# Kernel tuning notes

Measured on AMD Instinct MI355X. Metric: run time of the kernel, lower is better.

Reference implementation:

```python
import jax, jax.numpy as jnp
import numpy as np
from jax import lax

DN = ('NCHW', 'OIHW', 'NCHW')


def conv2d(x, w, b, stride, pad):
    y = lax.conv_general_dilated(x, w, (stride, stride), [(pad, pad), (pad, pad)],
                                 dimension_numbers=DN)
    return y + b[None, :, None, None]


def conv_transpose2d_k4s2p1(x, w, b):
    # torch ConvTranspose2d(k=4, s=2, p=1); w is torch layout [Cin, Cout, 4, 4].
    # Equivalent forward conv: lhs_dilation=2, pad = k-1-p = 2, spatially-flipped kernel.
    k = jnp.flip(w, (2, 3)).transpose(1, 0, 2, 3)  # -> OIHW [Cout, Cin, 4, 4]
    y = lax.conv_general_dilated(x, k, (1, 1), [(2, 2), (2, 2)],
                                 lhs_dilation=(2, 2), dimension_numbers=DN)
    return y + b[None, :, None, None]


def setup_inputs() -> dict:
    key = jax.random.key(0)
    ks = jax.random.split(key, 16)

    def w(k, shape):
        fan_in = int(np.prod(shape[1:]))
        return jax.random.normal(k, shape, jnp.float32) * np.float32(1.0 / np.sqrt(fan_in))

    inp = {}
    inp['x'] = jax.random.uniform(ks[0], (256, 1, 128, 128), jnp.float32)
    # Encoder
    inp['enc_w1'] = w(ks[1], (32, 1, 4, 4));   inp['enc_b1'] = jnp.zeros((32,), jnp.float32)
    inp['enc_w2'] = w(ks[2], (64, 32, 4, 4));  inp['enc_b2'] = jnp.zeros((64,), jnp.float32)
    inp['enc_w3'] = w(ks[3], (64, 64, 3, 3));  inp['enc_b3'] = jnp.zeros((64,), jnp.float32)
    inp['enc_w4'] = w(ks[4], (32, 64, 1, 1));  inp['enc_b4'] = jnp.zeros((32,), jnp.float32)
    # Codebook: uniform(-sqrt(3/512), sqrt(3/512))
    mx = np.float32(np.sqrt(3.0 / 512.0))
    inp['codebook'] = jax.random.uniform(ks[5], (512, 32), jnp.float32, -mx, mx)
    # Decoder
    inp['dec_w1'] = w(ks[6], (64, 32, 3, 3));  inp['dec_b1'] = jnp.zeros((64,), jnp.float32)
    inp['dect_w1'] = w(ks[7], (64, 32, 4, 4)); inp['dect_b1'] = jnp.zeros((32,), jnp.float32)  # torch [Cin,Cout,k,k]
    inp['dect_w2'] = w(ks[8], (32, 1, 4, 4));  inp['dect_b2'] = jnp.zeros((1,), jnp.float32)
    return inp


def vqvae_forward(x, enc_w1, enc_b1, enc_w2, enc_b2, enc_w3, enc_b3, enc_w4, enc_b4,
                  codebook, dec_w1, dec_b1, dect_w1, dect_b1, dect_w2, dect_b2):
    # Encoder: 128 -> 64 -> 32 spatial, 32 channels out
    h = jax.nn.relu(conv2d(x, enc_w1, enc_b1, 2, 1))
    h = jax.nn.relu(conv2d(h, enc_w2, enc_b2, 2, 1))
    h = jax.nn.relu(conv2d(h, enc_w3, enc_b3, 1, 1))
    z = conv2d(h, enc_w4, enc_b4, 1, 0)            # [B, 32, 32, 32]

    # Vector quantization (NCHW -> NHWC -> flat)
    zin = jnp.moveaxis(z, 1, -1)                   # [B, H, W, D]
    flat = zin.reshape(-1, zin.shape[-1])          # [N, D]
    dists = (jnp.sum(flat * flat, -1, keepdims=True)
             + jnp.sum(codebook * codebook, -1)
             - 2.0 * flat @ codebook.T)            # [N, K]
    idx = jnp.argmin(dists, -1)                    # [N]
    quant = codebook[idx].reshape(zin.shape)       # == one_hot @ codebook

    emb_loss = jnp.mean((quant - lax.stop_gradient(zin)) ** 2)
    com_loss = 0.26 * jnp.mean((lax.stop_gradient(quant) - zin) ** 2)
    vq_loss = emb_loss + com_loss
    quant = zin + lax.stop_gradient(quant - zin)   # straight-through
    qz = jnp.moveaxis(quant, -1, 1)                # [B, 32, 32, 32]

    # Decoder: 32 -> 64 -> 128 spatial
    d = jax.nn.relu(conv2d(qz, dec_w1, dec_b1, 1, 1))
    d = jax.nn.relu(conv_transpose2d_k4s2p1(d, dect_w1, dect_b1))
    recon = jax.nn.sigmoid(conv_transpose2d_k4s2p1(d, dect_w2, dect_b2))
    return recon, vq_loss


def reference(x, enc_w1, enc_b1, enc_w2, enc_b2, enc_w3, enc_b3, enc_w4, enc_b4,
              codebook, dec_w1, dec_b1, dect_w1, dect_b1, dect_w2, dect_b2):
    return vqvae_forward(x, enc_w1, enc_b1, enc_w2, enc_b2, enc_w3, enc_b3, enc_w4, enc_b4,
                         codebook, dec_w1, dec_b1, dect_w1, dect_b1, dect_w2, dect_b2)
```

## Files before the change

kernel.cpp:

```cpp
#include <hip/hip_runtime.h>
#include <math.h>

typedef __attribute__((ext_vector_type(8))) short short8;
typedef __attribute__((ext_vector_type(4))) float f32x4;

__device__ inline unsigned short f2bf(float f) {
  unsigned u = __float_as_uint(f);
  u = (u + 0x7fffu + ((u >> 16) & 1u)) >> 16;
  return (unsigned short)u;
}

__global__ __launch_bounds__(256, 3)
void conv1_lds(const float* __restrict__ x, const float* __restrict__ w,
               const float* __restrict__ bias, float* __restrict__ out) {
  int bid = blockIdx.x;
  int cchunk = bid & 1;
  int t4 = (bid >> 1) & 3;
  int n = bid >> 3;
  int co0 = cchunk * 16;
  int y0 = t4 * 16;
  int yi0 = 2 * y0 - 1;

  __shared__ float xs[34 * 128];
  __shared__ float wl[16][16];

  int t = threadIdx.x;
  for (int idx = t; idx < 34 * 128; idx += 256) {
    int gy = yi0 + (idx >> 7);
    int gx = idx & 127;
    bool ok = (unsigned)gy < 128;
    xs[idx] = ok ? x[(size_t)n * 16384 + gy * 128 + gx] : 0.f;
  }
  {
    int cc = t & 15;
    int tap = t >> 4;
    if (t < 256) wl[tap][cc] = w[(size_t)(co0 + cc) * 16 + tap];
  }
  __syncthreads();

  int sx = t & 63;
  int rg = t >> 6;

  float acc[4][16];
#pragma unroll
  for (int j = 0; j < 4; j++)
#pragma unroll
    for (int c = 0; c < 16; c++) acc[j][c] = 0.f;

  int ix0 = 2 * sx - 1;
#pragma unroll
  for (int ky = 0; ky < 4; ky++) {
#pragma unroll
    for (int kx = 0; kx < 4; kx++) {
      int ix = ix0 + kx;
      bool xok = (unsigned)ix < 128;
      float xv[4];
#pragma unroll
      for (int j = 0; j < 4; j++) {
        int lrow = 2 * (4 * rg + j) + ky;
        float v = xs[lrow * 128 + (xok ? ix : 0)];
        xv[j] = xok ? v : 0.f;
      }
      const float* wr = &wl[ky * 4 + kx][0];
#pragma unroll
      for (int c = 0; c < 16; c += 4) {
        float4 wv = *(const float4*)(wr + c);
#pragma unroll
        for (int j = 0; j < 4; j++) {
          acc[j][c + 0] = fmaf(xv[j], wv.x, acc[j][c + 0]);
          acc[j][c + 1] = fmaf(xv[j], wv.y, acc[j][c + 1]);
          acc[j][c + 2] = fmaf(xv[j], wv.z, acc[j][c + 2]);
          acc[j][c + 3] = fmaf(xv[j], wv.w, acc[j][c + 3]);
        }
      }
    }
  }

#pragma unroll
  for (int j = 0; j < 4; j++) {
    int oy = y0 + 4 * rg + j;
    float* op = out + (((size_t)n * 32 + co0) * 64 + oy) * 64 + sx;
#pragma unroll
    for (int c = 0; c < 16; c++) {
      float v = acc[j][c] + bias[co0 + c];
      op[(size_t)c * 4096] = fmaxf(v, 0.f);
    }
  }
}

template<int CIN, int COUT, int CCH>
__global__ __launch_bounds__(256, 3)
void conv4x4s2_lds(const float* __restrict__ x, const float* __restrict__ w,
                   const float* __restrict__ bias, float* __restrict__ out) {
  constexpr int NCH = COUT / CCH;
  int bid = blockIdx.x;
  int cchunk = bid % NCH;
  int n = bid / NCH;
  int co0 = cchunk * CCH;

  __shared__ float wl[CIN * 16][CCH];
  __shared__ float xs[4096];
  for (int i = threadIdx.x; i < CIN * 16 * CCH; i += 256) {
    int cc = i % CCH;
    int tap = i / CCH;
    wl[tap][cc] = w[(size_t)(co0 + cc) * (CIN * 16) + tap];
  }

  int t = threadIdx.x;
  int sx = t & 31;
  int sy0 = t >> 5;
  int ix0 = 2 * sx - 1;

  float acc[4][CCH];
#pragma unroll
  for (int j = 0; j < 4; j++)
#pragma unroll
    for (int c = 0; c < CCH; c++) acc[j][c] = 0.f;

  const float* xn = x + (size_t)n * CIN * 4096;

  for (int ci = 0; ci < CIN; ci++) {
    __syncthreads();
#pragma unroll
    for (int k = 0; k < 4; k++)
      *(float4*)(xs + k * 1024 + t * 4) =
          *(const float4*)(xn + (size_t)ci * 4096 + k * 1024 + t * 4);
    __syncthreads();

#pragma unroll
    for (int ky = 0; ky < 4; ky++) {
#pragma unroll
      for (int kx = 0; kx < 4; kx++) {
        int ix = ix0 + kx;
        bool xok = (unsigned)ix < 64;
        float xv[4];
#pragma unroll
        for (int j = 0; j < 4; j++) {
          int iy = 2 * (sy0 + j * 8) - 1 + ky;
          bool ok = xok && ((unsigned)iy < 64);
          float v = xs[ok ? iy * 64 + ix : 0];
          xv[j] = ok ? v : 0.f;
        }
        const float* wr = &wl[ci * 16 + ky * 4 + kx][0];
#pragma unroll
        for (int c = 0; c < CCH; c += 4) {
          float4 wv = *(const float4*)(wr + c);
#pragma unroll
          for (int j = 0; j < 4; j++) {
            acc[j][c + 0] = fmaf(xv[j], wv.x, acc[j][c + 0]);
            acc[j][c + 1] = fmaf(xv[j], wv.y, acc[j][c + 1]);
            acc[j][c + 2] = fmaf(xv[j], wv.z, acc[j][c + 2]);
            acc[j][c + 3] = fmaf(xv[j], wv.w, acc[j][c + 3]);
          }
        }
      }
    }
  }

#pragma unroll
  for (int j = 0; j < 4; j++) {
    int sy = sy0 + j * 8;
    float* op = out + (((size_t)n * COUT + co0) * 32 + sy) * 32 + sx;
#pragma unroll
    for (int c = 0; c < CCH; c++) {
      float v = acc[j][c] + bias[co0 + c];
      v = fmaxf(v, 0.f);
      op[(size_t)c * 1024] = v;
    }
  }
}

template<int CIN, int COUT, int CCH>
__global__ __launch_bounds__(256, 3)
void conv3x3_cg(const float* __restrict__ x, const float* __restrict__ w,
                const float* __restrict__ bias, float* __restrict__ out) {
  constexpr int NCH = COUT / CCH;
  int bid = blockIdx.x;
  int cchunk = bid % NCH;
  int n = bid / NCH;
  int co0 = cchunk * CCH;

  __shared__ float xs[4 * 1024];
  __shared__ float wl[4 * 9][CCH];

  int t = threadIdx.x;
  int sx = t & 31;
  int rg = t >> 5;

  float acc[4][CCH];
#pragma unroll
  for (int j = 0; j < 4; j++)
#pragma unroll
    for (int c = 0; c < CCH; c++) acc[j][c] = 0.f;

  const float* xn = x + (size_t)n * CIN * 1024;

  for (int cg = 0; cg < CIN / 4; cg++) {
    __syncthreads();
#pragma unroll
    for (int k = 0; k < 4; k++)
      *(float4*)(xs + k * 1024 + t * 4) =
          *(const float4*)(xn + (size_t)(cg * 4 + k) * 1024 + t * 4);
    for (int i = t; i < 4 * 9 * CCH; i += 256) {
      int cc = i % CCH;
      int row = i / CCH;
      int c4 = row / 9, kk = row % 9;
      wl[row][cc] = w[(size_t)(co0 + cc) * (CIN * 9) + (cg * 4 + c4) * 9 + kk];
    }
    __syncthreads();

#pragma unroll
    for (int c4 = 0; c4 < 4; c4++) {
      const float* xc = xs + c4 * 1024;
      float xv[6][3];
#pragma unroll
      for (int r = 0; r < 6; r++) {
        int iy = 4 * rg - 1 + r;
        bool yok = (unsigned)iy < 32;
#pragma unroll
        for (int cx = 0; cx < 3; cx++) {
          int ix = sx - 1 + cx;
          bool ok = yok && ((unsigned)ix < 32);
          float v = xc[ok ? iy * 32 + ix : 0];
          xv[r][cx] = ok ? v : 0.f;
        }
      }
#pragma unroll
      for (int ky = 0; ky < 3; ky++) {
#pragma unroll
        for (int kx = 0; kx < 3; kx++) {
          const float* wr = &wl[c4 * 9 + ky * 3 + kx][0];
#pragma unroll
          for (int c = 0; c < CCH; c += 4) {
            float4 wv = *(const float4*)(wr + c);
#pragma unroll
            for (int j = 0; j < 4; j++) {
              float xx = xv[j + ky][kx];
              acc[j][c + 0] = fmaf(xx, wv.x, acc[j][c + 0]);
              acc[j][c + 1] = fmaf(xx, wv.y, acc[j][c + 1]);
              acc[j][c + 2] = fmaf(xx, wv.z, acc[j][c + 2]);
              acc[j][c + 3] = fmaf(xx, wv.w, acc[j][c + 3]);
            }
          }
        }
      }
    }
  }

#pragma unroll
  for (int j = 0; j < 4; j++) {
    int sy = 4 * rg + j;
    float* op = out + (((size_t)n * COUT + co0) * 32 + sy) * 32 + sx;
#pragma unroll
    for (int c = 0; c < CCH; c++) {
      float v = acc[j][c] + bias[co0 + c];
      v = fmaxf(v, 0.f);
      op[(size_t)c * 1024] = v;
    }
  }
}

__global__ void wprep_dect1(const float* __restrict__ tw1,
                            unsigned short* __restrict__ Bws) {
  int i = blockIdx.x * 256 + threadIdx.x;
  if (i < 32768) {
    int ci = i & 63;
    int co = (i >> 6) & 31;
    int tap = (i >> 11) & 3;
    int par = i >> 13;
    int py = par >> 1, px = par & 1;
    int ky0 = (py + 1) & 1, kx0 = (px + 1) & 1;
    int kyi = tap >> 1, kxi = tap & 1;
    int ky = ky0 + 2 * kyi, kx = kx0 + 2 * kxi;
    Bws[i] = f2bf(tw1[(((size_t)ci * 32 + co) * 4 + ky) * 4 + kx]);
  }
}

__global__ void wprep_dec1(const float* __restrict__ dw1,
                           unsigned short* __restrict__ Wd1) {
  int i = blockIdx.x * 256 + threadIdx.x;
  if (i < 18432) {
    int ci = i & 31;
    int tap = (i >> 5) % 9;
    int co = i / 288;
    Wd1[i] = f2bf(dw1[(size_t)(co * 32 + ci) * 9 + tap]);
  }
}

__global__ __launch_bounds__(256, 3)
void dec1_mfma(const float* __restrict__ qz,
               const unsigned short* __restrict__ Wd1,
               const float* __restrict__ bias, float* __restrict__ d1) {
  int strip = blockIdx.x & 3;
  int smp = blockIdx.x >> 2;
  int y0 = strip * 8;

  __shared__ __align__(16) unsigned short xt[10 * 34 * 32];

  int t = threadIdx.x;
  for (int idx = t; idx < 16 * 10 * 34; idx += 256) {
    int cc = idx % 34;
    int tmp = idx / 34;
    int rr = tmp % 10;
    int pp = tmp / 10;
    int gy = y0 - 1 + rr;
    int gx = cc - 1;
    bool ok = ((unsigned)gy < 32) && ((unsigned)gx < 32);
    const float* p = qz + ((size_t)smp * 32 + 2 * pp) * 1024 + gy * 32 + gx;
    float v0 = ok ? p[0] : 0.f;
    float v1 = ok ? p[1024] : 0.f;
    unsigned pk = (unsigned)f2bf(v0) | ((unsigned)f2bf(v1) << 16);
    *(unsigned*)(&xt[(rr * 34 + cc) * 32 + 2 * pp]) = pk;
  }

  int lane = t & 63;
  int wv = t >> 6;
  int mlo = lane & 15;
  int khi = lane >> 4;

  short8 afr[9];
#pragma unroll
  for (int tap = 0; tap < 9; tap++)
    afr[tap] = *(const short8*)(Wd1 + (size_t)(wv * 16 + mlo) * 288 +
                                tap * 32 + khi * 8);
  float bb[4];
#pragma unroll
  for (int r = 0; r < 4; r++) bb[r] = bias[wv * 16 + khi * 4 + r];

  __syncthreads();

  for (int pt = 0; pt < 16; pt++) {
    int rl = pt >> 1;
    int chf = pt & 1;
    f32x4 acc = {0.f, 0.f, 0.f, 0.f};
#pragma unroll
    for (int tap = 0; tap < 9; tap++) {
      int ky = tap / 3, kx = tap % 3;
      const unsigned short* bp =
          xt + (((rl + ky) * 34) + chf * 16 + mlo + kx) * 32 + khi * 8;
      short8 b = *(const short8*)bp;
      acc = __builtin_amdgcn_mfma_f32_16x16x32_bf16(afr[tap], b, acc, 0, 0, 0);
    }
    int gyo = y0 + rl;
    int gxo = chf * 16 + mlo;
#pragma unroll
    for (int r = 0; r < 4; r++) {
      int co = wv * 16 + khi * 4 + r;
      d1[(((size_t)smp * 64 + co) * 32 + gyo) * 32 + gxo] =
          fmaxf(acc[r] + bb[r], 0.f);
    }
  }
}

__global__ __launch_bounds__(256, 3)
void convt_mfma(const float* __restrict__ d1,
                const unsigned short* __restrict__ Bws,
                const float* __restrict__ bias, float* __restrict__ d2) {
  constexpr int CP = 72;
  int bid = blockIdx.x;
  int rp = bid & 15;
  int smp = bid >> 4;

  __shared__ __align__(16) unsigned short xt[4 * 34 * CP];

  int t = threadIdx.x;

  for (int idx = t; idx < 32 * 4 * 34; idx += 256) {
    int cc = idx % 34;
    int tmp = idx / 34;
    int rr = tmp & 3;
    int pp = tmp >> 2;
    int gy = 2 * rp - 1 + rr;
    int gx = cc - 1;
    bool ok = ((unsigned)gy < 32) && ((unsigned)gx < 32);
    const float* p = d1 + ((size_t)smp * 64 + 2 * pp) * 1024 + gy * 32 + gx;
    float v0 = ok ? p[0] : 0.f;
    float v1 = ok ? p[1024] : 0.f;
    unsigned pk = (unsigned)f2bf(v0) | ((unsigned)f2bf(v1) << 16);
    *(unsigned*)(&xt[(rr * 34 + cc) * CP + 2 * pp]) = pk;
  }
  __syncthreads();

  int lane = t & 63;
  int wv = t >> 6;
  int row2 = wv >> 1;
  int c0 = (wv & 1) * 16;
  int mlo = lane & 15;
  int khi = lane >> 4;

  f32x4 acc[4][2];
#pragma unroll
  for (int par = 0; par < 4; par++)
#pragma unroll
    for (int nt = 0; nt < 2; nt++) {
      f32x4 z = {0.f, 0.f, 0.f, 0.f};
      acc[par][nt] = z;
    }

#pragma unroll
  for (int par = 0; par < 4; par++) {
    int py = par >> 1, px = par & 1;
    int ky0 = (py + 1) & 1, kx0 = (px + 1) & 1;
    int ay = (py + 1 - ky0) >> 1;
    int ax = (px + 1 - kx0) >> 1;
#pragma unroll
    for (int tap = 0; tap < 4; tap++) {
      int kyi = tap >> 1, kxi = tap & 1;
      int rrp = row2 + 1 + (ay - kyi);
      int ccb = c0 + 1 + (ax - kxi);
#pragma unroll
      for (int kc = 0; kc < 2; kc++) {
        const unsigned short* ap =
            xt + ((rrp * 34) + ccb + mlo) * CP + kc * 32 + khi * 8;
        short8 a = *(const short8*)ap;
#pragma unroll
        for (int nt = 0; nt < 2; nt++) {
          const unsigned short* bp =
              Bws + (((size_t)(par * 4 + tap) * 32 + nt * 16 + mlo) * 64) +
              kc * 32 + khi * 8;
          short8 b = *(const short8*)bp;
          acc[par][nt] =
              __builtin_amdgcn_mfma_f32_16x16x32_bf16(a, b, acc[par][nt], 0, 0, 0);
        }
      }
    }
  }

  int sy = 2 * rp + row2;
#pragma unroll
  for (int par = 0; par < 4; par++) {
    int py = par >> 1, px = par & 1;
    int oy = 2 * sy + py;
#pragma unroll
    for (int nt = 0; nt < 2; nt++) {
      int co = nt * 16 + mlo;
      float b = bias[co];
      float* op = d2 + (((size_t)smp * 32 + co) * 64 + oy) * 64;
#pragma unroll
      for (int r = 0; r < 4; r++) {
        int sx = c0 + khi * 4 + r;
        int ox = 2 * sx + px;
        op[ox] = fmaxf(acc[par][nt][r] + b, 0.f);
      }
    }
  }
}

__global__ __launch_bounds__(256, 4)
void dect2_full(const float* __restrict__ x, const float* __restrict__ w,
                const float* __restrict__ bias, float* __restrict__ out) {
  int ptile = blockIdx.x & 3;
  int n = blockIdx.x >> 2;
  int y0 = ptile * 16;

  __shared__ float xs[8][1152];
  int t = threadIdx.x;
  int sx = t & 63;
  int r4 = t >> 6;

  float acc[4][4];
#pragma unroll
  for (int j = 0; j < 4; j++)
#pragma unroll
    for (int p = 0; p < 4; p++) acc[j][p] = 0.f;

  const float* xn = x + (size_t)n * 32 * 4096;

  for (int cg = 0; cg < 4; cg++) {
    __syncthreads();
    for (int idx = t; idx < 8 * 1152; idx += 256) {
      int ch = idx / 1152;
      int rem = idx % 1152;
      int iy = y0 - 1 + rem / 64;
      int ix = rem & 63;
      bool ok = (unsigned)iy < 64;
      xs[ch][rem] = ok ? xn[(size_t)(cg * 8 + ch) * 4096 + iy * 64 + ix] : 0.f;
    }
    __syncthreads();

#pragma unroll
    for (int c4 = 0; c4 < 8; c4++) {
      int ci = cg * 8 + c4;
      const float* xc = &xs[c4][0];
      float xv[6][3];
#pragma unroll
      for (int r = 0; r < 6; r++) {
        int srow = 4 * r4 + r;
#pragma unroll
        for (int cx = 0; cx < 3; cx++) {
          int ix = sx - 1 + cx;
          bool ok = (unsigned)ix < 64;
          float v = xc[ok ? srow * 64 + ix : 0];
          xv[r][cx] = ok ? v : 0.f;
        }
      }
      float w16[16];
#pragma unroll
      for (int q = 0; q < 4; q++) {
        float4 ww = *(const float4*)(w + ci * 16 + 4 * q);
        w16[4 * q + 0] = ww.x; w16[4 * q + 1] = ww.y;
        w16[4 * q + 2] = ww.z; w16[4 * q + 3] = ww.w;
      }
#pragma unroll
      for (int py = 0; py < 2; py++) {
#pragma unroll
        for (int px = 0; px < 2; px++) {
          int par = py * 2 + px;
          int ky0 = (py + 1) & 1, kx0 = (px + 1) & 1;
          int ay = (py + 1 - ky0) >> 1;
          int ax = (px + 1 - kx0) >> 1;
#pragma unroll
          for (int kyi = 0; kyi < 2; kyi++) {
#pragma unroll
            for (int kxi = 0; kxi < 2; kxi++) {
              float wv = w16[(ky0 + 2 * kyi) * 4 + (kx0 + 2 * kxi)];
#pragma unroll
              for (int j = 0; j < 4; j++) {
                float xx = xv[j + ay + 1 - kyi][ax + 1 - kxi];
                acc[j][par] = fmaf(xx, wv, acc[j][par]);
              }
            }
          }
        }
      }
    }
  }

  float b0 = bias[0];
#pragma unroll
  for (int j = 0; j < 4; j++) {
    int iy = y0 + 4 * r4 + j;
#pragma unroll
    for (int py = 0; py < 2; py++) {
      float v0 = acc[j][py * 2 + 0] + b0;
      float v1 = acc[j][py * 2 + 1] + b0;
      float2 o;
      o.x = 1.f / (1.f + expf(-v0));
      o.y = 1.f / (1.f + expf(-v1));
      int oy = 2 * iy + py;
      *(float2*)(out + (size_t)n * 16384 + oy * 128 + 2 * sx) = o;
    }
  }
}

__global__ void cbn_prep(const float* __restrict__ cb, float* __restrict__ cbn) {
#pragma clang fp contract(off)
  int k = blockIdx.x * 256 + threadIdx.x;
  if (k < 512) {
    float m[32];
#pragma unroll
    for (int d = 0; d < 32; d++) {
      float c = cb[k * 32 + d];
      m[d] = c * c;
    }
    float r[8];
#pragma unroll
    for (int j = 0; j < 8; j++)
      r[j] = ((m[j] + m[8 + j]) + m[16 + j]) + m[24 + j];
    cbn[k] = ((r[0] + r[1]) + (r[2] + r[3])) + ((r[4] + r[5]) + (r[6] + r[7]));
  }
}

__global__ __launch_bounds__(256)
void vq_fused(const float* __restrict__ h3, const float* __restrict__ w4,
              const float* __restrict__ b4, const float* __restrict__ cb,
              const float* __restrict__ cbn, float* __restrict__ qz,
              float* __restrict__ loss) {
  __shared__ float wl[64][32];
  int tid = threadIdx.x;
  for (int i = tid; i < 2048; i += 256) {
    int co = i & 31;
    int ci = i >> 5;
    wl[ci][co] = w4[(size_t)co * 64 + ci];
  }
  __syncthreads();

  int n = blockIdx.x >> 2;
  int p = (blockIdx.x & 3) * 256 + tid;
  const float* hn = h3 + (size_t)n * 65536;

  float zv[32];
#pragma unroll
  for (int c = 0; c < 32; c++) zv[c] = 0.f;
  for (int ci = 0; ci < 64; ci++) {
    float xv = hn[(size_t)ci * 1024 + p];
#pragma unroll
    for (int c = 0; c < 32; c += 4) {
      float4 wv = *(const float4*)&wl[ci][c];
      zv[c + 0] = fmaf(xv, wv.x, zv[c + 0]);
      zv[c + 1] = fmaf(xv, wv.y, zv[c + 1]);
      zv[c + 2] = fmaf(xv, wv.z, zv[c + 2]);
      zv[c + 3] = fmaf(xv, wv.w, zv[c + 3]);
    }
  }
#pragma unroll
  for (int c = 0; c < 32; c++) zv[c] = zv[c] + b4[c];

  float zz;
  {
#pragma clang fp contract(off)
    float m[32];
#pragma unroll
    for (int d = 0; d < 32; d++) m[d] = zv[d] * zv[d];
    float r[8];
#pragma unroll
    for (int j = 0; j < 8; j++)
      r[j] = ((m[j] + m[8 + j]) + m[16 + j]) + m[24 + j];
    zz = ((r[0] + r[1]) + (r[2] + r[3])) + ((r[4] + r[5]) + (r[6] + r[7]));
  }

  float best = 3.4e38f;
  int bk = 0;
  for (int k4 = 0; k4 < 512; k4 += 4) {
    float4 cn = *(const float4*)(cbn + k4);
    float da[4];
#pragma unroll
    for (int u = 0; u < 4; u++) da[u] = 0.f;
#pragma unroll
    for (int d = 0; d < 32; d += 4) {
#pragma unroll
      for (int u = 0; u < 4; u++) {
        float4 c = *(const float4*)(cb + (size_t)(k4 + u) * 32 + d);
        float a = da[u];
        a = fmaf(zv[d + 0], c.x, a);
        a = fmaf(zv[d + 1], c.y, a);
        a = fmaf(zv[d + 2], c.z, a);
        a = fmaf(zv[d + 3], c.w, a);
        da[u] = a;
      }
    }
#pragma unroll
    for (int u = 0; u < 4; u++) {
      float cnu = (u == 0) ? cn.x : (u == 1) ? cn.y : (u == 2) ? cn.z : cn.w;
      float s;
      {
#pragma clang fp contract(off)
        s = (zz + cnu) - 2.f * da[u];
      }
      int k = k4 + u;
      if (s < best) { best = s; bk = k; }
    }
  }

  float lsum = 0.f;
  float* qn = qz + (size_t)n * 32768;
#pragma unroll
  for (int d = 0; d < 32; d += 4) {
#pragma clang fp contract(off)
    float4 q = *(const float4*)(cb + (size_t)bk * 32 + d);
    float e;
    e = q.x - zv[d + 0]; lsum = fmaf(e, e, lsum);
    e = q.y - zv[d + 1]; lsum = fmaf(e, e, lsum);
    e = q.z - zv[d + 2]; lsum = fmaf(e, e, lsum);
    e = q.w - zv[d + 3]; lsum = fmaf(e, e, lsum);
    qn[(size_t)(d + 0) * 1024 + p] = zv[d + 0] + (q.x - zv[d + 0]);
    qn[(size_t)(d + 1) * 1024 + p] = zv[d + 1] + (q.y - zv[d + 1]);
    qn[(size_t)(d + 2) * 1024 + p] = zv[d + 2] + (q.z - zv[d + 2]);
    qn[(size_t)(d + 3) * 1024 + p] = zv[d + 3] + (q.w - zv[d + 3]);
  }

#pragma unroll
  for (int off = 32; off; off >>= 1) lsum += __shfl_down(lsum, off, 64);
  if ((tid & 63) == 0) atomicAdd(loss, lsum);
}

__global__ void finalize_loss(const float* __restrict__ loss, float* __restrict__ out) {
  if (threadIdx.x == 0) {
    float m = loss[0] / 8388608.f;
    out[0] = m + 0.26f * m;
  }
}

extern "C" void kernel_launch(void* const* d_in, const int* in_sizes, int n_in,
                              void* d_out, int out_size, void* d_ws, size_t ws_size,
                              hipStream_t stream) {
  (void)in_sizes; (void)n_in; (void)out_size;
  const float* x   = (const float*)d_in[0];
  const float* ew1 = (const float*)d_in[1];
  const float* eb1 = (const float*)d_in[2];
  const float* ew2 = (const float*)d_in[3];
  const float* eb2 = (const float*)d_in[4];
  const float* ew3 = (const float*)d_in[5];
  const float* eb3 = (const float*)d_in[6];
  const float* ew4 = (const float*)d_in[7];
  const float* eb4 = (const float*)d_in[8];
  const float* cb  = (const float*)d_in[9];
  const float* dw1 = (const float*)d_in[10];
  const float* db1 = (const float*)d_in[11];
  const float* tw1 = (const float*)d_in[12];
  const float* tb1 = (const float*)d_in[13];
  const float* tw2 = (const float*)d_in[14];
  const float* tb2 = (const float*)d_in[15];
  float* out = (float*)d_out;

  auto need = [](size_t c) -> size_t {
    return (c * 196608 + 516 + 16384 + 9216) * 4;
  };
  int nchunks = 4;
  if (ws_size >= need(256)) nchunks = 1;
  else if (ws_size >= need(128)) nchunks = 2;
  int chunk = 256 / nchunks;

  float* ws = (float*)d_ws;
  float* A = ws;
  float* B = A + (size_t)chunk * 131072;
  float* cbn = B + (size_t)chunk * 65536;
  float* lossacc = cbn + 512;
  unsigned short* Bws = (unsigned short*)(cbn + 516);
  unsigned short* Wd1 = (unsigned short*)(cbn + 516 + 16384);

  float* h1 = A;
  float* h2 = B;
  float* h3 = A;
  float* qz = A + (size_t)chunk * 98304;
  float* d1 = B;
  float* d2 = A;

  cbn_prep<<<2, 256, 0, stream>>>(cb, cbn);
  wprep_dect1<<<128, 256, 0, stream>>>(tw1, Bws);
  wprep_dec1<<<72, 256, 0, stream>>>(dw1, Wd1);
  (void)hipMemsetAsync(lossacc, 0, 4, stream);

  for (int c = 0; c < nchunks; c++) {
    const float* xc = x + (size_t)c * chunk * 128 * 128;
    float* outc = out + (size_t)c * chunk * 128 * 128;

    conv1_lds<<<chunk * 8, 256, 0, stream>>>(xc, ew1, eb1, h1);
    conv4x4s2_lds<32, 64, 16>
        <<<chunk * 4, 256, 0, stream>>>(h1, ew2, eb2, h2);
    conv3x3_cg<64, 64, 16>
        <<<chunk * 4, 256, 0, stream>>>(h2, ew3, eb3, h3);

    vq_fused<<<chunk * 4, 256, 0, stream>>>(h3, ew4, eb4, cb, cbn, qz, lossacc);

    dec1_mfma<<<chunk * 4, 256, 0, stream>>>(qz, Wd1, db1, d1);
    convt_mfma<<<chunk * 16, 256, 0, stream>>>(d1, Bws, tb1, d2);
    dect2_full<<<chunk * 4, 256, 0, stream>>>(d2, tw2, tb2, outc);
  }

  finalize_loss<<<1, 64, 0, stream>>>(lossacc, out + 4194304);
}
```

Baseline: 1.085 ms.

## Enlarge per-block channel tile and per-thread register tile in encoder convs

The two middle encoder convolutions now give each block 32 output channels instead of 16, with each thread holding an 8-row by 16-channel accumulator tile, which halves the grid. Each staged input tile is therefore reused across twice as many output channels, and loaded weights across more rows, cutting global and LDS traffic per FMA. The 4x4 conv now stages only the current input channel's weights into a small LDS array each iteration instead of the whole weight slice up front. In exchange, register pressure rises (launch bounds drop to 2 blocks per SM) and the grid has fewer blocks, which lowers occupancy and latency hiding.

```diff
diff --git a/kernel.cpp b/kernel.cpp
--- a/kernel.cpp
+++ b/kernel.cpp
@@ -88,34 +88,30 @@
   }
 }
 
-template<int CIN, int COUT, int CCH>
-__global__ __launch_bounds__(256, 3)
-void conv4x4s2_lds(const float* __restrict__ x, const float* __restrict__ w,
-                   const float* __restrict__ bias, float* __restrict__ out) {
-  constexpr int NCH = COUT / CCH;
+template<int CIN, int COUT>
+__global__ __launch_bounds__(256, 2)
+void conv4x4s2_v2(const float* __restrict__ x, const float* __restrict__ w,
+                  const float* __restrict__ bias, float* __restrict__ out) {
+  constexpr int NCH = COUT / 32;
   int bid = blockIdx.x;
   int cchunk = bid % NCH;
   int n = bid / NCH;
-  int co0 = cchunk * CCH;
-
-  __shared__ float wl[CIN * 16][CCH];
+  int co0 = cchunk * 32;
+
   __shared__ float xs[4096];
-  for (int i = threadIdx.x; i < CIN * 16 * CCH; i += 256) {
-    int cc = i % CCH;
-    int tap = i / CCH;
-    wl[tap][cc] = w[(size_t)(co0 + cc) * (CIN * 16) + tap];
-  }
+  __shared__ float wl[16][32];
 
   int t = threadIdx.x;
   int sx = t & 31;
-  int sy0 = t >> 5;
+  int rg = (t >> 5) & 3;
+  int cob = (t >> 7) * 16;
   int ix0 = 2 * sx - 1;
 
-  float acc[4][CCH];
-#pragma unroll
-  for (int j = 0; j < 4; j++)
-#pragma unroll
-    for (int c = 0; c < CCH; c++) acc[j][c] = 0.f;
+  float acc[8][16];
+#pragma unroll
+  for (int j = 0; j < 8; j++)
+#pragma unroll
+    for (int c = 0; c < 16; c++) acc[j][c] = 0.f;
 
   const float* xn = x + (size_t)n * CIN * 4096;
 
@@ -125,6 +121,14 @@
     for (int k = 0; k < 4; k++)
       *(float4*)(xs + k * 1024 + t * 4) =
           *(const float4*)(xn + (size_t)ci * 4096 + k * 1024 + t * 4);
+    {
+      int i = t;
+      int cc = i & 31, tap = i >> 5;
+      wl[tap][cc] = w[(size_t)(co0 + cc) * (CIN * 16) + ci * 16 + tap];
+      i += 256;
+      cc = i & 31; tap = i >> 5;
+      wl[tap][cc] = w[(size_t)(co0 + cc) * (CIN * 16) + ci * 16 + tap];
+    }
     __syncthreads();
 
 #pragma unroll
@@ -133,20 +137,20 @@
       for (int kx = 0; kx < 4; kx++) {
         int ix = ix0 + kx;
         bool xok = (unsigned)ix < 64;
-        float xv[4];
-#pragma unroll
-        for (int j = 0; j < 4; j++) {
-          int iy = 2 * (sy0 + j * 8) - 1 + ky;
+        float xv[8];
+#pragma unroll
+        for (int j = 0; j < 8; j++) {
+          int iy = 2 * (8 * rg + j) - 1 + ky;
           bool ok = xok && ((unsigned)iy < 64);
           float v = xs[ok ? iy * 64 + ix : 0];
           xv[j] = ok ? v : 0.f;
         }
-        const float* wr = &wl[ci * 16 + ky * 4 + kx][0];
-#pragma unroll
-        for (int c = 0; c < CCH; c += 4) {
+        const float* wr = &wl[ky * 4 + kx][cob];
+#pragma unroll
+        for (int c = 0; c < 16; c += 4) {
           float4 wv = *(const float4*)(wr + c);
 #pragma unroll
-          for (int j = 0; j < 4; j++) {
+          for (int j = 0; j < 8; j++) {
             acc[j][c + 0] = fmaf(xv[j], wv.x, acc[j][c + 0]);
             acc[j][c + 1] = fmaf(xv[j], wv.y, acc[j][c + 1]);
             acc[j][c + 2] = fmaf(xv[j], wv.z, acc[j][c + 2]);
@@ -158,40 +162,40 @@
   }
 
 #pragma unroll
-  for (int j = 0; j < 4; j++) {
-    int sy = sy0 + j * 8;
-    float* op = out + (((size_t)n * COUT + co0) * 32 + sy) * 32 + sx;
-#pragma unroll
-    for (int c = 0; c < CCH; c++) {
-      float v = acc[j][c] + bias[co0 + c];
-      v = fmaxf(v, 0.f);
-      op[(size_t)c * 1024] = v;
-    }
-  }
-}
-
-template<int CIN, int COUT, int CCH>
-__global__ __launch_bounds__(256, 3)
-void conv3x3_cg(const float* __restrict__ x, const float* __restrict__ w,
+  for (int j = 0; j < 8; j++) {
+    int sy = 8 * rg + j;
+    float* op = out + (((size_t)n * COUT + co0 + cob) * 32 + sy) * 32 + sx;
+#pragma unroll
+    for (int c = 0; c < 16; c++) {
+      float v = acc[j][c] + bias[co0 + cob + c];
+      op[(size_t)c * 1024] = fmaxf(v, 0.f);
+    }
+  }
+}
+
+template<int CIN, int COUT>
+__global__ __launch_bounds__(256, 2)
+void conv3x3_v2(const float* __restrict__ x, const float* __restrict__ w,
                 const float* __restrict__ bias, float* __restrict__ out) {
-  constexpr int NCH = COUT / CCH;
+  constexpr int NCH = COUT / 32;
   int bid = blockIdx.x;
   int cchunk = bid % NCH;
   int n = bid / NCH;
-  int co0 = cchunk * CCH;
+  int co0 = cchunk * 32;
 
   __shared__ float xs[4 * 1024];
-  __shared__ float wl[4 * 9][CCH];
+  __shared__ float wl[4 * 9][32];
 
   int t = threadIdx.x;
   int sx = t & 31;
-  int rg = t >> 5;
-
-  float acc[4][CCH];
-#pragma unroll
-  for (int j = 0; j < 4; j++)
-#pragma unroll
-    for (int c = 0; c < CCH; c++) acc[j][c] = 0.f;
+  int rg = (t >> 5) & 3;
+  int cob = (t >> 7) * 16;
+
+  float acc[8][16];
+#pragma unroll
+  for (int j = 0; j < 8; j++)
+#pragma unroll
+    for (int c = 0; c < 16; c++) acc[j][c] = 0.f;
 
   const float* xn = x + (size_t)n * CIN * 1024;
 
@@ -201,9 +205,9 @@
     for (int k = 0; k < 4; k++)
       *(float4*)(xs + k * 1024 + t * 4) =
           *(const float4*)(xn + (size_t)(cg * 4 + k) * 1024 + t * 4);
-    for (int i = t; i < 4 * 9 * CCH; i += 256) {
-      int cc = i % CCH;
-      int row = i / CCH;
+    for (int i = t; i < 4 * 9 * 32; i += 256) {
+      int cc = i & 31;
+      int row = i >> 5;
       int c4 = row / 9, kk = row % 9;
       wl[row][cc] = w[(size_t)(co0 + cc) * (CIN * 9) + (cg * 4 + c4) * 9 + kk];
     }
@@ -212,10 +216,10 @@
 #pragma unroll
     for (int c4 = 0; c4 < 4; c4++) {
       const float* xc = xs + c4 * 1024;
-      float xv[6][3];
-#pragma unroll
-      for (int r = 0; r < 6; r++) {
-        int iy = 4 * rg - 1 + r;
+      float xv[10][3];
+#pragma unroll
+      for (int r = 0; r < 10; r++) {
+        int iy = 8 * rg - 1 + r;
         bool yok = (unsigned)iy < 32;
 #pragma unroll
         for (int cx = 0; cx < 3; cx++) {
@@ -229,12 +233,12 @@
       for (int ky = 0; ky < 3; ky++) {
 #pragma unroll
         for (int kx = 0; kx < 3; kx++) {
-          const float* wr = &wl[c4 * 9 + ky * 3 + kx][0];
-#pragma unroll
-          for (int c = 0; c < CCH; c += 4) {
+          const float* wr = &wl[c4 * 9 + ky * 3 + kx][cob];
+#pragma unroll
+          for (int c = 0; c < 16; c += 4) {
             float4 wv = *(const float4*)(wr + c);
 #pragma unroll
-            for (int j = 0; j < 4; j++) {
+            for (int j = 0; j < 8; j++) {
               float xx = xv[j + ky][kx];
               acc[j][c + 0] = fmaf(xx, wv.x, acc[j][c + 0]);
               acc[j][c + 1] = fmaf(xx, wv.y, acc[j][c + 1]);
@@ -248,14 +252,13 @@
   }
 
 #pragma unroll
-  for (int j = 0; j < 4; j++) {
-    int sy = 4 * rg + j;
-    float* op = out + (((size_t)n * COUT + co0) * 32 + sy) * 32 + sx;
-#pragma unroll
-    for (int c = 0; c < CCH; c++) {
-      float v = acc[j][c] + bias[co0 + c];
-      v = fmaxf(v, 0.f);
-      op[(size_t)c * 1024] = v;
+  for (int j = 0; j < 8; j++) {
+    int sy = 8 * rg + j;
+    float* op = out + (((size_t)n * COUT + co0 + cob) * 32 + sy) * 32 + sx;
+#pragma unroll
+    for (int c = 0; c < 16; c++) {
+      float v = acc[j][c] + bias[co0 + cob + c];
+      op[(size_t)c * 1024] = fmaxf(v, 0.f);
     }
   }
 }
@@ -726,10 +729,10 @@
     float* outc = out + (size_t)c * chunk * 128 * 128;
 
     conv1_lds<<<chunk * 8, 256, 0, stream>>>(xc, ew1, eb1, h1);
-    conv4x4s2_lds<32, 64, 16>
-        <<<chunk * 4, 256, 0, stream>>>(h1, ew2, eb2, h2);
-    conv3x3_cg<64, 64, 16>
-        <<<chunk * 4, 256, 0, stream>>>(h2, ew3, eb3, h3);
+    conv4x4s2_v2<32, 64>
+        <<<chunk * 2, 256, 0, stream>>>(h1, ew2, eb2, h2);
+    conv3x3_v2<64, 64>
+        <<<chunk * 2, 256, 0, stream>>>(h2, ew3, eb3, h3);
 
     vq_fused<<<chunk * 4, 256, 0, stream>>>(h3, ew4, eb4, cb, cbn, qz, lossacc);
 
```

Result: slower. 1.432 ms (+32.0%).

## Pad LDS halos, stream per-channel weights, raise occupancy bounds

Applied to the files above, without the earlier changes.

The conv4x4 encoder kernel now loads weights one input channel at a time into a small LDS tile instead of staging all CIN*16*CCH weights up front. Both encoder convs gain zeroed halo rows in LDS, so vertical bounds checks drop out of the inner loops. Launch bounds on several kernels go from 3 to 4 blocks per CU. The aim is lower LDS and register pressure for higher occupancy and cheaper indexing, at the cost of per-iteration weight loads from global memory and possible register spills under the tighter bound.

```diff
diff --git a/kernel.cpp b/kernel.cpp
--- a/kernel.cpp
+++ b/kernel.cpp
@@ -10,7 +10,7 @@
   return (unsigned short)u;
 }
 
-__global__ __launch_bounds__(256, 3)
+__global__ __launch_bounds__(256, 4)
 void conv1_lds(const float* __restrict__ x, const float* __restrict__ w,
                const float* __restrict__ bias, float* __restrict__ out) {
   int bid = blockIdx.x;
@@ -89,28 +89,28 @@
 }
 
 template<int CIN, int COUT, int CCH>
-__global__ __launch_bounds__(256, 3)
-void conv4x4s2_lds(const float* __restrict__ x, const float* __restrict__ w,
-                   const float* __restrict__ bias, float* __restrict__ out) {
+__global__ __launch_bounds__(256, 4)
+void conv4x4s2_h4(const float* __restrict__ x, const float* __restrict__ w,
+                  const float* __restrict__ bias, float* __restrict__ out) {
   constexpr int NCH = COUT / CCH;
   int bid = blockIdx.x;
   int cchunk = bid % NCH;
   int n = bid / NCH;
   int co0 = cchunk * CCH;
 
-  __shared__ float wl[CIN * 16][CCH];
-  __shared__ float xs[4096];
-  for (int i = threadIdx.x; i < CIN * 16 * CCH; i += 256) {
-    int cc = i % CCH;
-    int tap = i / CCH;
-    wl[tap][cc] = w[(size_t)(co0 + cc) * (CIN * 16) + tap];
-  }
+  __shared__ float xs[66 * 64];
+  __shared__ float wl[16][CCH];
 
   int t = threadIdx.x;
   int sx = t & 31;
   int sy0 = t >> 5;
   int ix0 = 2 * sx - 1;
 
+  if (t < 128) {
+    int r = (t >> 6) ? 65 : 0;
+    xs[r * 64 + (t & 63)] = 0.f;
+  }
+
   float acc[4][CCH];
 #pragma unroll
   for (int j = 0; j < 4; j++)
@@ -122,9 +122,18 @@
   for (int ci = 0; ci < CIN; ci++) {
     __syncthreads();
 #pragma unroll
-    for (int k = 0; k < 4; k++)
-      *(float4*)(xs + k * 1024 + t * 4) =
-          *(const float4*)(xn + (size_t)ci * 4096 + k * 1024 + t * 4);
+    for (int k = 0; k < 4; k++) {
+      int idx = k * 1024 + t * 4;
+      int row = idx >> 6;
+      int col = idx & 63;
+      *(float4*)(xs + (row + 1) * 64 + col) =
+          *(const float4*)(xn + (size_t)ci * 4096 + idx);
+    }
+    {
+      int cc = t & (CCH - 1);
+      int tap = t >> 4;
+      if (tap < 16) wl[tap][cc] = w[(size_t)(co0 + cc) * (CIN * 16) + ci * 16 + tap];
+    }
     __syncthreads();
 
 #pragma unroll
@@ -133,15 +142,15 @@
       for (int kx = 0; kx < 4; kx++) {
         int ix = ix0 + kx;
         bool xok = (unsigned)ix < 64;
+        int ixs = xok ? ix : 0;
         float xv[4];
 #pragma unroll
         for (int j = 0; j < 4; j++) {
-          int iy = 2 * (sy0 + j * 8) - 1 + ky;
-          bool ok = xok && ((unsigned)iy < 64);
-          float v = xs[ok ? iy * 64 + ix : 0];
-          xv[j] = ok ? v : 0.f;
+          int row = 2 * (sy0 + j * 8) + ky;
+          float v = xs[row * 64 + ixs];
+          xv[j] = xok ? v : 0.f;
         }
-        const float* wr = &wl[ci * 16 + ky * 4 + kx][0];
+        const float* wr = &wl[ky * 4 + kx][0];
 #pragma unroll
         for (int c = 0; c < CCH; c += 4) {
           float4 wv = *(const float4*)(wr + c);
@@ -171,8 +180,8 @@
 }
 
 template<int CIN, int COUT, int CCH>
-__global__ __launch_bounds__(256, 3)
-void conv3x3_cg(const float* __restrict__ x, const float* __restrict__ w,
+__global__ __launch_bounds__(256, 4)
+void conv3x3_h4(const float* __restrict__ x, const float* __restrict__ w,
                 const float* __restrict__ bias, float* __restrict__ out) {
   constexpr int NCH = COUT / CCH;
   int bid = blockIdx.x;
@@ -180,13 +189,20 @@
   int n = bid / NCH;
   int co0 = cchunk * CCH;
 
-  __shared__ float xs[4 * 1024];
+  __shared__ float xs[4][34 * 32];
   __shared__ float wl[4 * 9][CCH];
 
   int t = threadIdx.x;
   int sx = t & 31;
   int rg = t >> 5;
 
+  {
+    int p = t >> 6;
+    int idx = t & 63;
+    int row = (idx >> 5) ? 33 : 0;
+    xs[p][row * 32 + (idx & 31)] = 0.f;
+  }
+
   float acc[4][CCH];
 #pragma unroll
   for (int j = 0; j < 4; j++)
@@ -198,9 +214,12 @@
   for (int cg = 0; cg < CIN / 4; cg++) {
     __syncthreads();
 #pragma unroll
-    for (int k = 0; k < 4; k++)
-      *(float4*)(xs + k * 1024 + t * 4) =
+    for (int k = 0; k < 4; k++) {
+      int row = t >> 3;
+      int col = (t & 7) * 4;
+      *(float4*)(&xs[k][(row + 1) * 32 + col]) =
           *(const float4*)(xn + (size_t)(cg * 4 + k) * 1024 + t * 4);
+    }
     for (int i = t; i < 4 * 9 * CCH; i += 256) {
       int cc = i % CCH;
       int row = i / CCH;
@@ -211,18 +230,17 @@
 
 #pragma unroll
     for (int c4 = 0; c4 < 4; c4++) {
-      const float* xc = xs + c4 * 1024;
+      const float* xc = &xs[c4][0];
       float xv[6][3];
 #pragma unroll
-      for (int r = 0; r < 6; r++) {
-        int iy = 4 * rg - 1 + r;
-        bool yok = (unsigned)iy < 32;
-#pragma unroll
-        for (int cx = 0; cx < 3; cx++) {
-          int ix = sx - 1 + cx;
-          bool ok = yok && ((unsigned)ix < 32);
-          float v = xc[ok ? iy * 32 + ix : 0];
-          xv[r][cx] = ok ? v : 0.f;
+      for (int cx = 0; cx < 3; cx++) {
+        int ix = sx - 1 + cx;
+        bool xok = (unsigned)ix < 32;
+        int ixs = xok ? ix : 0;
+#pragma unroll
+        for (int r = 0; r < 6; r++) {
+          float v = xc[(4 * rg + r) * 32 + ixs];
+          xv[r][cx] = xok ? v : 0.f;
         }
       }
 #pragma unroll
@@ -287,7 +305,7 @@
   }
 }
 
-__global__ __launch_bounds__(256, 3)
+__global__ __launch_bounds__(256, 4)
 void dec1_mfma(const float* __restrict__ qz,
                const unsigned short* __restrict__ Wd1,
                const float* __restrict__ bias, float* __restrict__ d1) {
@@ -352,7 +370,7 @@
   }
 }
 
-__global__ __launch_bounds__(256, 3)
+__global__ __launch_bounds__(256, 4)
 void convt_mfma(const float* __restrict__ d1,
                 const unsigned short* __restrict__ Bws,
                 const float* __restrict__ bias, float* __restrict__ d2) {
@@ -726,9 +744,9 @@
     float* outc = out + (size_t)c * chunk * 128 * 128;
 
     conv1_lds<<<chunk * 8, 256, 0, stream>>>(xc, ew1, eb1, h1);
-    conv4x4s2_lds<32, 64, 16>
+    conv4x4s2_h4<32, 64, 16>
         <<<chunk * 4, 256, 0, stream>>>(h1, ew2, eb2, h2);
-    conv3x3_cg<64, 64, 16>
+    conv3x3_h4<64, 64, 16>
         <<<chunk * 4, 256, 0, stream>>>(h2, ew3, eb3, h3);
 
     vq_fused<<<chunk * 4, 256, 0, stream>>>(h3, ew4, eb4, cb, cbn, qz, lossacc);
```

New measurement: 1.084 ms. Within noise of the previous version (-0.1%).
